# Performance work log

Measured on AMD Instinct MI355X. Metric: run time of the kernel, lower is better.

## Reference

```python
import jax, jax.numpy as jnp
import numpy as np


def setup_inputs() -> dict:
    key = jax.random.key(0)
    kq, kk, kv = jax.random.split(key, 3)
    B, L, H, D = 2, 4096, 8, 64
    queries = jax.random.normal(kq, (B, L, H, D), dtype=jnp.float32)
    keys = jax.random.normal(kk, (B, L, H, D), dtype=jnp.float32)
    values = jax.random.normal(kv, (B, L, H, D), dtype=jnp.float32)
    return {"queries": queries, "keys": keys, "values": values}


def reference(queries, keys, values):
    # queries/keys/values: [B, L, H, D]
    d_model = queries.shape[-1]
    scale = 1.0 / jnp.sqrt(jnp.asarray(d_model, dtype=queries.dtype))
    # scores: [B, H, Lq, Lk]
    scores = jnp.einsum('blhd,bshd->bhls', queries, keys)
    # dropout is identity in eval mode / for deterministic reference
    A = jax.nn.softmax(scale * scores, axis=-1)
    # output: [B, Lq, H, D]
    V = jnp.einsum('bhls,bshd->blhd', A, values)
    return V
```

## Files before the change

### kernel.cpp

```cpp
#include <hip/hip_runtime.h>

#define Bn 2
#define Ln 4096
#define Hn 8
#define Dn 64
#define NMEGA 32
#define BH_STRIDE 262144

typedef float    f32x4  __attribute__((ext_vector_type(4)));
typedef float    f32x16 __attribute__((ext_vector_type(16)));
typedef _Float16 f16x2  __attribute__((ext_vector_type(2)));
typedef _Float16 f16x8  __attribute__((ext_vector_type(8)));
typedef unsigned int u32;
typedef u32 u32x2 __attribute__((ext_vector_type(2)));
typedef u32 u32x4 __attribute__((ext_vector_type(4)));

static __device__ __forceinline__ u32 pkf16(float a, float b){
    auto h = __builtin_amdgcn_cvt_pkrtz(a, b);
    return __builtin_bit_cast(u32, h);
}

static __device__ __forceinline__ u32x2 swp(u32 a, u32 b){
    auto r = __builtin_amdgcn_permlane32_swap(a, b, false, false);
    return __builtin_bit_cast(u32x2, r);
}

__global__ __launch_bounds__(256)
void kvprep(const float* __restrict__ Kg, const float* __restrict__ Vg,
            _Float16* __restrict__ kp, _Float16* __restrict__ vp){
    __shared__ float tV[64*65];
    const int t = blockIdx.x, bh = blockIdx.y, b = bh>>3, h = bh&7;
    const int tid = threadIdx.x;
#pragma unroll
    for(int i=0;i<4;++i){
        int idx = tid + i*256;
        int k = idx >> 4, d4 = (idx & 15)*4;
        float4 v = *(const float4*)(Vg + (((size_t)b*Ln + t*64 + k)*Hn + h)*Dn + d4);
        tV[k*65+d4+0]=v.x; tV[k*65+d4+1]=v.y;
        tV[k*65+d4+2]=v.z; tV[k*65+d4+3]=v.w;
    }
#pragma unroll
    for(int i=0;i<2;++i){
        int u = tid + i*256;
        int lane = u & 63, unit = u >> 6;
        int g = unit >> 2, cc = unit & 3;
        const float* src = Kg + (((size_t)b*Ln + t*64 + g*32 + (lane&31))*Hn + h)*Dn
                         + cc*16 + (lane>>5)*8;
        float4 a = *(const float4*)src;
        float4 c4 = *(const float4*)(src + 4);
        f16x8 o;
        o[0]=(_Float16)a.x;  o[1]=(_Float16)a.y;  o[2]=(_Float16)a.z;  o[3]=(_Float16)a.w;
        o[4]=(_Float16)c4.x; o[5]=(_Float16)c4.y; o[6]=(_Float16)c4.z; o[7]=(_Float16)c4.w;
        *(f16x8*)(kp + (size_t)bh*BH_STRIDE + (size_t)t*4096 + (size_t)u*8) = o;
    }
    __syncthreads();
#pragma unroll
    for(int i=0;i<2;++i){
        int u = tid + i*256;
        int lane = u & 63, unit = u >> 6;
        int g = unit >> 2, kh = (unit >> 1) & 1, dt = unit & 1;
        int krow = g*32 + kh*16 + (lane>>5)*8;
        int d = dt*32 + (lane&31);
        f16x8 o;
#pragma unroll
        for(int j=0;j<8;++j) o[j] = (_Float16)tV[(krow+j)*65 + d];
        *(f16x8*)(vp + (size_t)bh*BH_STRIDE + (size_t)t*4096 + (size_t)u*8) = o;
    }
}

static __device__ __forceinline__ f32x16 qk4(const f16x8 kf[4], const f16x8 qf[4]){
    f32x16 s;
#pragma unroll
    for(int r=0;r<16;++r) s[r]=0.f;
    s = __builtin_amdgcn_mfma_f32_32x32x16_f16(kf[0], qf[0], s, 0,0,0);
    s = __builtin_amdgcn_mfma_f32_32x32x16_f16(kf[1], qf[1], s, 0,0,0);
    s = __builtin_amdgcn_mfma_f32_32x32x16_f16(kf[2], qf[2], s, 0,0,0);
    s = __builtin_amdgcn_mfma_f32_32x32x16_f16(kf[3], qf[3], s, 0,0,0);
    return s;
}

static __device__ __forceinline__ void finish_pv(const f32x16& S, float& lac,
                                                 f32x16& o0, f32x16& o1,
                                                 const f16x8 vf[4]){
    f32x16 p;
#pragma unroll
    for(int r=0;r<16;++r) p[r] = __builtin_amdgcn_exp2f(S[r]);
    u32 A0 = pkf16(p[0],p[1]),   A1 = pkf16(p[2],p[3]);
    u32 B0 = pkf16(p[4],p[5]),   B1 = pkf16(p[6],p[7]);
    u32 C0 = pkf16(p[8],p[9]),   C1 = pkf16(p[10],p[11]);
    u32 D0 = pkf16(p[12],p[13]), D1 = pkf16(p[14],p[15]);
    u32x2 r0 = swp(A0,B0), r1 = swp(A1,B1);
    u32x2 r2 = swp(C0,D0), r3 = swp(C1,D1);
    u32x4 w0 = {r0.x, r1.x, r0.y, r1.y};
    u32x4 w1 = {r2.x, r3.x, r2.y, r3.y};
    f16x8 pa0 = __builtin_bit_cast(f16x8, w0);
    f16x8 pa1 = __builtin_bit_cast(f16x8, w1);
    const f16x2 ones = {(_Float16)1.0f, (_Float16)1.0f};
#pragma unroll
    for(int j=0;j<4;++j){
        f16x2 c0 = {pa0[2*j], pa0[2*j+1]};
        f16x2 c1 = {pa1[2*j], pa1[2*j+1]};
        lac = __builtin_amdgcn_fdot2(c0, ones, lac, false);
        lac = __builtin_amdgcn_fdot2(c1, ones, lac, false);
    }
    o0 = __builtin_amdgcn_mfma_f32_32x32x16_f16(pa0, vf[0], o0, 0,0,0);
    o0 = __builtin_amdgcn_mfma_f32_32x32x16_f16(pa1, vf[2], o0, 0,0,0);
    o1 = __builtin_amdgcn_mfma_f32_32x32x16_f16(pa0, vf[1], o1, 0,0,0);
    o1 = __builtin_amdgcn_mfma_f32_32x32x16_f16(pa1, vf[3], o1, 0,0,0);
}

__global__ __launch_bounds__(256,2)
void attn_fwd(const float* __restrict__ Qg, float* __restrict__ Og,
              const _Float16* __restrict__ kp, const _Float16* __restrict__ vp){
    __shared__ __align__(16) float xo[128*68 + 128];

    const int tid  = threadIdx.x;
    const int lane = tid & 63, wv = tid >> 6;
    const int qh = wv & 1, kh2 = wv >> 1;
    const int l31 = lane & 31, hi = lane >> 5;
    const int bh = blockIdx.x, b = bh>>3, h = bh&7;
    const int q0 = blockIdx.y*128 + qh*64;

    const float c = 0.125f * 1.4426950408889634f;

    f16x8 qf[2][4];
#pragma unroll
    for(int qt=0;qt<2;++qt){
        const float* qrow = Qg + (((size_t)b*Ln + q0 + qt*32 + l31)*Hn + h)*Dn;
#pragma unroll
        for(int cc=0;cc<4;++cc){
            const float* p4 = qrow + cc*16 + hi*8;
            float4 x = *(const float4*)p4;
            float4 y = *(const float4*)(p4+4);
            f16x8 f;
            f[0]=(_Float16)(x.x*c); f[1]=(_Float16)(x.y*c);
            f[2]=(_Float16)(x.z*c); f[3]=(_Float16)(x.w*c);
            f[4]=(_Float16)(y.x*c); f[5]=(_Float16)(y.y*c);
            f[6]=(_Float16)(y.z*c); f[7]=(_Float16)(y.w*c);
            qf[qt][cc]=f;
        }
    }

    f32x16 o[2][2];
    float lac[2] = {0.f, 0.f};
#pragma unroll
    for(int qt=0;qt<2;++qt)
#pragma unroll
        for(int dt=0;dt<2;++dt)
#pragma unroll
            for(int r=0;r<16;++r) o[qt][dt][r]=0.f;

    const char* kgc = (const char*)(kp + (size_t)bh*BH_STRIDE) + kh2*8192 + lane*16;
    const char* vgc = (const char*)(vp + (size_t)bh*BH_STRIDE) + kh2*8192 + lane*16;

    for(int T=0; T<NMEGA; ++T){
        const char* Kb = kgc + (size_t)T*16384;
        const char* Vb = vgc + (size_t)T*16384;

        f16x8 kf0[4], vf0[4];
#pragma unroll
        for(int cc=0;cc<4;++cc) kf0[cc] = *(const f16x8*)(Kb + (cc<<10));
#pragma unroll
        for(int j=0;j<4;++j)    vf0[j]  = *(const f16x8*)(Vb + (j<<10));

        f32x16 S0 = qk4(kf0, qf[0]);
        f32x16 S1 = qk4(kf0, qf[1]);

        f16x8 kf1[4], vf1[4];
#pragma unroll
        for(int cc=0;cc<4;++cc) kf1[cc] = *(const f16x8*)(Kb + ((4+cc)<<10));
#pragma unroll
        for(int j=0;j<4;++j)    vf1[j]  = *(const f16x8*)(Vb + ((4+j)<<10));

        finish_pv(S0, lac[0], o[0][0], o[0][1], vf0);
        f32x16 S0b = qk4(kf1, qf[0]);
        finish_pv(S1, lac[1], o[1][0], o[1][1], vf0);
        f32x16 S1b = qk4(kf1, qf[1]);
        finish_pv(S0b, lac[0], o[0][0], o[0][1], vf1);
        finish_pv(S1b, lac[1], o[1][0], o[1][1], vf1);
    }

    float lred[2];
#pragma unroll
    for(int qt=0;qt<2;++qt)
        lred[qt] = lac[qt] + __shfl_xor(lac[qt], 32, 64);

    float* xl = xo + 128*68;
    if(kh2){
#pragma unroll
        for(int qt=0;qt<2;++qt){
#pragma unroll
            for(int dt=0;dt<2;++dt)
#pragma unroll
                for(int r=0;r<16;++r){
                    int qr = (r&3) + 8*(r>>2) + 4*hi;
                    xo[(qh*64 + qt*32 + qr)*68 + dt*32 + l31] = o[qt][dt][r];
                }
            if(hi==0) xl[qh*64 + qt*32 + l31] = lred[qt];
        }
    }
    __syncthreads();
    if(!kh2){
#pragma unroll
        for(int qt=0;qt<2;++qt){
            float inv = 1.0f/(lred[qt] + xl[qh*64 + qt*32 + l31]);
            float* ob = Og + (((size_t)b*Ln + q0 + qt*32)*Hn + h)*Dn;
#pragma unroll
            for(int r=0;r<16;++r){
                int qr = (r&3) + 8*(r>>2) + 4*hi;
                float invr = __shfl(inv, qr, 64);
#pragma unroll
                for(int dt=0;dt<2;++dt){
                    float val = o[qt][dt][r] + xo[(qh*64 + qt*32 + qr)*68 + dt*32 + l31];
                    ob[(size_t)qr*Hn*Dn + dt*32 + l31] = val*invr;
                }
            }
        }
    }
}

extern "C" void kernel_launch(void* const* d_in, const int* in_sizes, int n_in,
                              void* d_out, int out_size, void* d_ws, size_t ws_size,
                              hipStream_t stream) {
    const float* Q = (const float*)d_in[0];
    const float* K = (const float*)d_in[1];
    const float* V = (const float*)d_in[2];
    float* O = (float*)d_out;

    _Float16* kp = (_Float16*)d_ws;
    _Float16* vp = (_Float16*)((char*)d_ws + (8u<<20));

    kvprep<<<dim3(64, 16), dim3(256), 0, stream>>>(K, V, kp, vp);
    attn_fwd<<<dim3(16, 32), dim3(256), 0, stream>>>(Q, O, kp, vp);
}
```

Before: 162.7 us.

## Double-buffer K/V register fragments with one-iteration-ahead prefetch

The K/V fragment loads for the next mega-tile are issued while the current tile's QK and PV MFMAs run. Registers are ping-ponged between X and Y buffer sets, and the loop is unrolled by two. Launch bounds drop from two blocks per CU to one so the doubled fragment registers fit. This hides global-load latency inside compute at the cost of occupancy, and the last iteration makes a redundant load of tile 0.

```diff
diff --git a/kernel.cpp b/kernel.cpp
--- a/kernel.cpp
+++ b/kernel.cpp
@@ -68,7 +68,7 @@
     }
 }
 
-static __device__ __forceinline__ f32x16 qk4(const f16x8 kf[4], const f16x8 qf[4]){
+static __device__ __forceinline__ f32x16 qk4(const f16x8 (&kf)[4], const f16x8 (&qf)[4]){
     f32x16 s;
 #pragma unroll
     for(int r=0;r<16;++r) s[r]=0.f;
@@ -81,7 +81,7 @@
 
 static __device__ __forceinline__ void finish_pv(const f32x16& S, float& lac,
                                                  f32x16& o0, f32x16& o1,
-                                                 const f16x8 vf[4]){
+                                                 const f16x8 (&vf)[4]){
     f32x16 p;
 #pragma unroll
     for(int r=0;r<16;++r) p[r] = __builtin_amdgcn_exp2f(S[r]);
@@ -109,7 +109,12 @@
     o1 = __builtin_amdgcn_mfma_f32_32x32x16_f16(pa1, vf[3], o1, 0,0,0);
 }
 
-__global__ __launch_bounds__(256,2)
+static __device__ __forceinline__ void ld4(f16x8 (&dst)[4], const char* base, int off){
+#pragma unroll
+    for(int i=0;i<4;++i) dst[i] = *(const f16x8*)(base + ((off+i)<<10));
+}
+
+__global__ __launch_bounds__(256,1)
 void attn_fwd(const float* __restrict__ Qg, float* __restrict__ Og,
               const _Float16* __restrict__ kp, const _Float16* __restrict__ vp){
     __shared__ __align__(16) float xo[128*68 + 128];
@@ -153,32 +158,38 @@
     const char* kgc = (const char*)(kp + (size_t)bh*BH_STRIDE) + kh2*8192 + lane*16;
     const char* vgc = (const char*)(vp + (size_t)bh*BH_STRIDE) + kh2*8192 + lane*16;
 
-    for(int T=0; T<NMEGA; ++T){
-        const char* Kb = kgc + (size_t)T*16384;
-        const char* Vb = vgc + (size_t)T*16384;
-
-        f16x8 kf0[4], vf0[4];
-#pragma unroll
-        for(int cc=0;cc<4;++cc) kf0[cc] = *(const f16x8*)(Kb + (cc<<10));
-#pragma unroll
-        for(int j=0;j<4;++j)    vf0[j]  = *(const f16x8*)(Vb + (j<<10));
-
-        f32x16 S0 = qk4(kf0, qf[0]);
-        f32x16 S1 = qk4(kf0, qf[1]);
-
-        f16x8 kf1[4], vf1[4];
-#pragma unroll
-        for(int cc=0;cc<4;++cc) kf1[cc] = *(const f16x8*)(Kb + ((4+cc)<<10));
-#pragma unroll
-        for(int j=0;j<4;++j)    vf1[j]  = *(const f16x8*)(Vb + ((4+j)<<10));
-
-        finish_pv(S0, lac[0], o[0][0], o[0][1], vf0);
-        f32x16 S0b = qk4(kf1, qf[0]);
-        finish_pv(S1, lac[1], o[1][0], o[1][1], vf0);
-        f32x16 S1b = qk4(kf1, qf[1]);
-        finish_pv(S0b, lac[0], o[0][0], o[0][1], vf1);
-        finish_pv(S1b, lac[1], o[1][0], o[1][1], vf1);
-    }
+    f16x8 kXA[4], vXA[4], kXB[4], vXB[4];
+    f16x8 kYA[4], vYA[4], kYB[4], vYB[4];
+
+    ld4(kXA, kgc, 0); ld4(vXA, vgc, 0);
+    ld4(kXB, kgc, 4); ld4(vXB, vgc, 4);
+
+#define BODY(kA,vA,kB,vB, nkA,nvA,nkB,nvB, KbN,VbN)                      \
+    {                                                                    \
+        ld4(nkA, KbN, 0);                                                \
+        f32x16 S0 = qk4(kA, qf[0]);                                      \
+        f32x16 S1 = qk4(kA, qf[1]);                                      \
+        ld4(nvA, VbN, 0);                                                \
+        finish_pv(S0, lac[0], o[0][0], o[0][1], vA);                     \
+        f32x16 S0b = qk4(kB, qf[0]);                                     \
+        ld4(nkB, KbN, 4);                                                \
+        finish_pv(S1, lac[1], o[1][0], o[1][1], vA);                     \
+        f32x16 S1b = qk4(kB, qf[1]);                                     \
+        ld4(nvB, VbN, 4);                                                \
+        finish_pv(S0b, lac[0], o[0][0], o[0][1], vB);                    \
+        finish_pv(S1b, lac[1], o[1][0], o[1][1], vB);                    \
+    }
+
+    for(int T=0; T<NMEGA; T+=2){
+        const char* KbY = kgc + (size_t)(T+1)*16384;
+        const char* VbY = vgc + (size_t)(T+1)*16384;
+        BODY(kXA,vXA,kXB,vXB, kYA,vYA,kYB,vYB, KbY,VbY);
+        const int Tn = (T+2 < NMEGA) ? (T+2) : 0;
+        const char* KbX = kgc + (size_t)Tn*16384;
+        const char* VbX = vgc + (size_t)Tn*16384;
+        BODY(kYA,vYA,kYB,vYB, kXA,vXA,kXB,vXB, KbX,VbX);
+    }
+#undef BODY
 
     float lred[2];
 #pragma unroll
```

Result: slower. 174.4 us (+7.2%).

## Split attention work across 8 waves with 32 query rows each

Applied to the files above, without the earlier changes.

The attention kernel grows from 4 to 8 waves per block. Each wave now handles one 32-row query tile instead of two, and the key dimension is still split in halves across wave pairs. This halves per-wave accumulator registers and raises wave-level parallelism, which should help latency hiding. In exchange, each K/V fragment loaded from global memory is reused for only one query tile instead of two, so load traffic per MFMA doubles.

```diff
diff --git a/kernel.cpp b/kernel.cpp
--- a/kernel.cpp
+++ b/kernel.cpp
@@ -68,7 +68,7 @@
     }
 }
 
-static __device__ __forceinline__ f32x16 qk4(const f16x8 kf[4], const f16x8 qf[4]){
+static __device__ __forceinline__ f32x16 qk4(const f16x8 (&kf)[4], const f16x8 (&qf)[4]){
     f32x16 s;
 #pragma unroll
     for(int r=0;r<16;++r) s[r]=0.f;
@@ -81,7 +81,7 @@
 
 static __device__ __forceinline__ void finish_pv(const f32x16& S, float& lac,
                                                  f32x16& o0, f32x16& o1,
-                                                 const f16x8 vf[4]){
+                                                 const f16x8 (&vf)[4]){
     f32x16 p;
 #pragma unroll
     for(int r=0;r<16;++r) p[r] = __builtin_amdgcn_exp2f(S[r]);
@@ -109,24 +109,28 @@
     o1 = __builtin_amdgcn_mfma_f32_32x32x16_f16(pa1, vf[3], o1, 0,0,0);
 }
 
-__global__ __launch_bounds__(256,2)
+static __device__ __forceinline__ void ld4(f16x8 (&dst)[4], const char* base, int off){
+#pragma unroll
+    for(int i=0;i<4;++i) dst[i] = *(const f16x8*)(base + ((off+i)<<10));
+}
+
+__global__ __launch_bounds__(512,2)
 void attn_fwd(const float* __restrict__ Qg, float* __restrict__ Og,
               const _Float16* __restrict__ kp, const _Float16* __restrict__ vp){
-    __shared__ __align__(16) float xo[128*68 + 128];
+    __shared__ __align__(16) float xo[4*32*64 + 128];
 
     const int tid  = threadIdx.x;
     const int lane = tid & 63, wv = tid >> 6;
-    const int qh = wv & 1, kh2 = wv >> 1;
+    const int kh2 = wv & 1, qh = wv >> 1;
     const int l31 = lane & 31, hi = lane >> 5;
     const int bh = blockIdx.x, b = bh>>3, h = bh&7;
-    const int q0 = blockIdx.y*128 + qh*64;
+    const int q0 = blockIdx.y*128 + qh*32;
 
     const float c = 0.125f * 1.4426950408889634f;
 
-    f16x8 qf[2][4];
-#pragma unroll
-    for(int qt=0;qt<2;++qt){
-        const float* qrow = Qg + (((size_t)b*Ln + q0 + qt*32 + l31)*Hn + h)*Dn;
+    f16x8 qf[4];
+    {
+        const float* qrow = Qg + (((size_t)b*Ln + q0 + l31)*Hn + h)*Dn;
 #pragma unroll
         for(int cc=0;cc<4;++cc){
             const float* p4 = qrow + cc*16 + hi*8;
@@ -137,18 +141,14 @@
             f[2]=(_Float16)(x.z*c); f[3]=(_Float16)(x.w*c);
             f[4]=(_Float16)(y.x*c); f[5]=(_Float16)(y.y*c);
             f[6]=(_Float16)(y.z*c); f[7]=(_Float16)(y.w*c);
-            qf[qt][cc]=f;
+            qf[cc]=f;
         }
     }
 
-    f32x16 o[2][2];
-    float lac[2] = {0.f, 0.f};
-#pragma unroll
-    for(int qt=0;qt<2;++qt)
-#pragma unroll
-        for(int dt=0;dt<2;++dt)
-#pragma unroll
-            for(int r=0;r<16;++r) o[qt][dt][r]=0.f;
+    f32x16 o0, o1;
+    float lac = 0.f;
+#pragma unroll
+    for(int r=0;r<16;++r){ o0[r]=0.f; o1[r]=0.f; }
 
     const char* kgc = (const char*)(kp + (size_t)bh*BH_STRIDE) + kh2*8192 + lane*16;
     const char* vgc = (const char*)(vp + (size_t)bh*BH_STRIDE) + kh2*8192 + lane*16;
@@ -158,63 +158,41 @@
         const char* Vb = vgc + (size_t)T*16384;
 
         f16x8 kf0[4], vf0[4];
-#pragma unroll
-        for(int cc=0;cc<4;++cc) kf0[cc] = *(const f16x8*)(Kb + (cc<<10));
-#pragma unroll
-        for(int j=0;j<4;++j)    vf0[j]  = *(const f16x8*)(Vb + (j<<10));
-
-        f32x16 S0 = qk4(kf0, qf[0]);
-        f32x16 S1 = qk4(kf0, qf[1]);
+        ld4(kf0, Kb, 0); ld4(vf0, Vb, 0);
+        f32x16 S0 = qk4(kf0, qf);
 
         f16x8 kf1[4], vf1[4];
-#pragma unroll
-        for(int cc=0;cc<4;++cc) kf1[cc] = *(const f16x8*)(Kb + ((4+cc)<<10));
-#pragma unroll
-        for(int j=0;j<4;++j)    vf1[j]  = *(const f16x8*)(Vb + ((4+j)<<10));
-
-        finish_pv(S0, lac[0], o[0][0], o[0][1], vf0);
-        f32x16 S0b = qk4(kf1, qf[0]);
-        finish_pv(S1, lac[1], o[1][0], o[1][1], vf0);
-        f32x16 S1b = qk4(kf1, qf[1]);
-        finish_pv(S0b, lac[0], o[0][0], o[0][1], vf1);
-        finish_pv(S1b, lac[1], o[1][0], o[1][1], vf1);
-    }
-
-    float lred[2];
-#pragma unroll
-    for(int qt=0;qt<2;++qt)
-        lred[qt] = lac[qt] + __shfl_xor(lac[qt], 32, 64);
-
-    float* xl = xo + 128*68;
+        ld4(kf1, Kb, 4); ld4(vf1, Vb, 4);
+        finish_pv(S0, lac, o0, o1, vf0);
+
+        f32x16 S1 = qk4(kf1, qf);
+        finish_pv(S1, lac, o0, o1, vf1);
+    }
+
+    float lred = lac + __shfl_xor(lac, 32, 64);
+
+    float* xl = xo + 4*32*64;
     if(kh2){
 #pragma unroll
-        for(int qt=0;qt<2;++qt){
-#pragma unroll
-            for(int dt=0;dt<2;++dt)
-#pragma unroll
-                for(int r=0;r<16;++r){
-                    int qr = (r&3) + 8*(r>>2) + 4*hi;
-                    xo[(qh*64 + qt*32 + qr)*68 + dt*32 + l31] = o[qt][dt][r];
-                }
-            if(hi==0) xl[qh*64 + qt*32 + l31] = lred[qt];
+        for(int r=0;r<16;++r){
+            int qr = (r&3) + 8*(r>>2) + 4*hi;
+            xo[(qh*32 + qr)*64 +  0 + l31] = o0[r];
+            xo[(qh*32 + qr)*64 + 32 + l31] = o1[r];
         }
+        if(hi==0) xl[qh*32 + l31] = lred;
     }
     __syncthreads();
     if(!kh2){
-#pragma unroll
-        for(int qt=0;qt<2;++qt){
-            float inv = 1.0f/(lred[qt] + xl[qh*64 + qt*32 + l31]);
-            float* ob = Og + (((size_t)b*Ln + q0 + qt*32)*Hn + h)*Dn;
-#pragma unroll
-            for(int r=0;r<16;++r){
-                int qr = (r&3) + 8*(r>>2) + 4*hi;
-                float invr = __shfl(inv, qr, 64);
-#pragma unroll
-                for(int dt=0;dt<2;++dt){
-                    float val = o[qt][dt][r] + xo[(qh*64 + qt*32 + qr)*68 + dt*32 + l31];
-                    ob[(size_t)qr*Hn*Dn + dt*32 + l31] = val*invr;
-                }
-            }
+        float inv = 1.0f/(lred + xl[qh*32 + l31]);
+        float* ob = Og + (((size_t)b*Ln + q0)*Hn + h)*Dn;
+#pragma unroll
+        for(int r=0;r<16;++r){
+            int qr = (r&3) + 8*(r>>2) + 4*hi;
+            float invr = __shfl(inv, qr, 64);
+            float v0 = o0[r] + xo[(qh*32 + qr)*64 +  0 + l31];
+            float v1 = o1[r] + xo[(qh*32 + qr)*64 + 32 + l31];
+            ob[(size_t)qr*Hn*Dn +  0 + l31] = v0*invr;
+            ob[(size_t)qr*Hn*Dn + 32 + l31] = v1*invr;
         }
     }
 }
@@ -231,5 +209,5 @@
     _Float16* vp = (_Float16*)((char*)d_ws + (8u<<20));
 
     kvprep<<<dim3(64, 16), dim3(256), 0, stream>>>(K, V, kp, vp);
-    attn_fwd<<<dim3(16, 32), dim3(256), 0, stream>>>(Q, O, kp, vp);
-}
+    attn_fwd<<<dim3(16, 32), dim3(512), 0, stream>>>(Q, O, kp, vp);
+}
```

Result: slower. 202.5 us (+24.5%).
